# Optimization experiments

Measured on AMD Instinct MI355X. Metric: run time of the kernel, lower is better.

Reference implementation:

```python
import jax, jax.numpy as jnp
import numpy as np
import math

B, T, C, D, E = 4, 2048, 2048, 128, 16

def _xavier(key, shape):
    fan_in, fan_out = shape[-2], shape[-1]
    a = math.sqrt(6.0 / (fan_in + fan_out))
    return jax.random.uniform(key, shape, jnp.float32, -a, a)

def setup_inputs() -> dict:
    key = jax.random.key(0)
    ks = jax.random.split(key, 6)
    return {
        'hidden_states': jax.random.normal(ks[0], (B, T, C), jnp.float32),
        'sim_matrix': jax.random.normal(ks[1], (C, E), jnp.float32),
        'gates': jnp.zeros((E,), jnp.float32),
        'q_proj': _xavier(ks[2], (E, C, D)),
        'k_proj': _xavier(ks[3], (E, C, D)),
        'v_proj': _xavier(ks[4], (E, C, D)),
        'o_proj': _xavier(ks[5], (E, D, C)),
        'min_experts': 2,
    }

def _gating(hidden_states, sim_matrix, gates, min_experts):
    b, t, c = hidden_states.shape
    e = sim_matrix.shape[1]
    x = hidden_states.reshape(b * t, c)
    xn = x / jnp.maximum(jnp.linalg.norm(x, axis=-1, keepdims=True), 1e-12)
    sn = sim_matrix / jnp.maximum(jnp.linalg.norm(sim_matrix, axis=0, keepdims=True), 1e-12)
    logits = xn @ sn - jax.nn.sigmoid(gates)            # [N, E]
    gated = jax.nn.relu(logits)
    # STE: hard threshold forward, identity backward
    hard = (gated > 0).astype(gated.dtype)
    act_mask = gated + jax.lax.stop_gradient(hard - gated)
    inactive = jnp.sum(act_mask, axis=1) == 0           # [N]
    _, fb_idx = jax.lax.top_k(logits, min_experts)      # [N, k]
    fb_mask = jnp.max(jax.nn.one_hot(fb_idx, e, dtype=act_mask.dtype), axis=1)
    act_mask = jnp.where(inactive[:, None], jnp.maximum(act_mask, fb_mask), act_mask)
    masked = jnp.where(act_mask > 0, gated, -jnp.inf)
    routing = jax.nn.softmax(masked, axis=-1)
    return routing.reshape(b, t, e)

def reference(hidden_states, sim_matrix, gates, q_proj, k_proj, v_proj, o_proj, min_experts):
    b, t, c = hidden_states.shape
    rw = _gating(hidden_states, sim_matrix, gates, min_experts)   # [B,T,E]
    # fused: per-expert GEMM then routing-weighted sum (avoids [B,T,D,C] weight tensor)
    q = jnp.einsum('bte,bted->btd', rw, jnp.einsum('btc,ecd->bted', hidden_states, q_proj))
    k = jnp.einsum('bte,bted->btd', rw, jnp.einsum('btc,ecd->bted', hidden_states, k_proj))
    v = jnp.einsum('bte,bted->btd', rw, jnp.einsum('btc,ecd->bted', hidden_states, v_proj))
    scale = 1.0 / math.sqrt(q.shape[-1])
    scores = jnp.einsum('btd,bsd->bts', q, k) * scale
    causal = jnp.tril(jnp.ones((t, t), bool))
    scores = jnp.where(causal[None], scores, -jnp.inf)
    attn = jax.nn.softmax(scores, axis=-1)
    o = jnp.einsum('bts,bsd->btd', attn, v)                       # [B,T,D]
    # output projection: weighted per-expert o_proj applied per token
    out = jnp.einsum('bte,bted->btd'.replace('d','c'), rw, jnp.einsum('btd,edc->btec', o, o_proj))
    return out
```

## Files before the change

### kernel.cpp

```cpp
#include <hip/hip_runtime.h>
#include <hip/hip_bf16.h>

#define DEV __device__ __forceinline__

typedef short bf16x8 __attribute__((ext_vector_type(8)));
typedef float f32x4 __attribute__((ext_vector_type(4)));
typedef unsigned short u16x4 __attribute__((ext_vector_type(4)));

static constexpr int Bsz = 4, Tt = 2048, Cch = 2048, Dd = 128, Ee = 16;
static constexpr int Nn = Bsz * Tt;
static constexpr int CAP = 1280;
static constexpr int MAXTILES = 320;
static constexpr int MT = CAP / 128;
static constexpr int NGRP = MT * Ee;

DEV unsigned short f2bf(float v) {
    __hip_bfloat16 h = __float2bfloat16(v);
    return __builtin_bit_cast(unsigned short, h);
}
DEV float bf2f(unsigned short u) {
    unsigned int x = ((unsigned int)u) << 16;
    return __builtin_bit_cast(float, x);
}

__global__ __launch_bounds__(256) void simt_kernel(const float* __restrict__ sim,
                                                   float* __restrict__ simT) {
    int i = blockIdx.x * 256 + threadIdx.x;
    int e = i >> 11, c = i & 2047;
    simT[i] = sim[c * 16 + e];
}

__global__ __launch_bounds__(1024) void gating6_kernel(
    const float* __restrict__ x, const float* __restrict__ simT,
    const float* __restrict__ gates, const int* __restrict__ minex,
    float* __restrict__ rw, unsigned short* __restrict__ xb,
    int* __restrict__ onmaskv) {
    __shared__ f32x4 ssim[8192];
    __shared__ float snv[16];
    const int tid = threadIdx.x;
    const f32x4* stg = (const f32x4*)simT;
#pragma unroll
    for (int i = 0; i < 8; i++) ssim[i * 1024 + tid] = stg[i * 1024 + tid];
    __syncthreads();
    const int wave = tid >> 6, lane = tid & 63;

    {
        float s = 0.f;
#pragma unroll
        for (int it = 0; it < 8; it++) {
            const f32x4 v = ssim[wave * 512 + it * 64 + lane];
            s += v[0] * v[0] + v[1] * v[1] + v[2] * v[2] + v[3] * v[3];
        }
#pragma unroll
        for (int off = 32; off; off >>= 1) s += __shfl_down(s, off);
        if (lane == 0) snv[wave] = 1.f / fmaxf(sqrtf(s), 1e-12f);
    }
    __syncthreads();

#pragma unroll 1
    for (int g = 0; g < 2; g++) {
        const int n = blockIdx.x * 32 + g * 16 + wave;
        const f32x4* xr = (const f32x4*)(x + (size_t)n * Cch);
        u16x4* xbr = (u16x4*)(xb + (size_t)n * Cch);
        float ss = 0.f;
        float d[16];
#pragma unroll
        for (int e = 0; e < 16; e++) d[e] = 0.f;

#pragma unroll 2
        for (int it = 0; it < 8; it++) {
            const int i = it * 64 + lane;
            const f32x4 xv = xr[i];
            ss += xv[0] * xv[0] + xv[1] * xv[1] + xv[2] * xv[2] + xv[3] * xv[3];
            u16x4 xc = {f2bf(xv[0]), f2bf(xv[1]), f2bf(xv[2]), f2bf(xv[3])};
            xbr[i] = xc;
#pragma unroll
            for (int e = 0; e < 16; e++) {
                const f32x4 sv = ssim[e * 512 + i];
                d[e] += xv[0] * sv[0] + xv[1] * sv[1] + xv[2] * sv[2] + xv[3] * sv[3];
            }
        }
#pragma unroll
        for (int off = 32; off; off >>= 1) {
            ss += __shfl_down(ss, off);
#pragma unroll
            for (int e = 0; e < 16; e++) d[e] += __shfl_down(d[e], off);
        }
        if (lane == 0) {
            float inv = 1.f / fmaxf(sqrtf(ss), 1e-12f);
            float logit[16];
            int onmask = 0;
#pragma unroll
            for (int e = 0; e < 16; e++) {
                float sg = 1.f / (1.f + __expf(-gates[e]));
                float l = d[e] * inv * snv[e] - sg;
                logit[e] = l;
                if (l > 0.f) onmask |= (1 << e);
            }
            if (onmask == 0) {
                int k = *minex;
                int ch = 0;
                for (int kk = 0; kk < k; kk++) {
                    float bv = -1e30f;
                    int be = 0;
#pragma unroll
                    for (int e = 0; e < 16; e++)
                        if (!((ch >> e) & 1) && logit[e] > bv) { bv = logit[e]; be = e; }
                    ch |= (1 << be);
                }
                onmask = ch;
            }
            float mx = -1e30f;
#pragma unroll
            for (int e = 0; e < 16; e++)
                if ((onmask >> e) & 1) mx = fmaxf(mx, fmaxf(logit[e], 0.f));
            float pe[16];
            float sum = 0.f;
#pragma unroll
            for (int e = 0; e < 16; e++) {
                pe[e] = ((onmask >> e) & 1) ? __expf(fmaxf(logit[e], 0.f) - mx) : 0.f;
                sum += pe[e];
            }
            float isum = 1.f / sum;
#pragma unroll
            for (int e = 0; e < 16; e++) rw[(size_t)n * 16 + e] = pe[e] * isum;
            onmaskv[n] = onmask;
        }
    }
}

__global__ __launch_bounds__(256) void scan_fused(
    const int* __restrict__ onmaskv,
    int* __restrict__ idx, int* __restrict__ pos, int* __restrict__ cnt,
    int* __restrict__ ptok, int4* __restrict__ tiledesc, int* __restrict__ ntile_dev,
    int* __restrict__ ocnt, int* __restrict__ olist) {
    const int tid = threadIdx.x;
    const int lane = tid & 63, w = tid >> 6;
    if (blockIdx.x < 16) {
        const int e = blockIdx.x;
        const int base = tid * 32;
        int om[32];
        int c = 0;
#pragma unroll
        for (int i = 0; i < 32; i++) {
            om[i] = (onmaskv[base + i] >> e) & 1;
            c += om[i];
        }
        int sc = c;
#pragma unroll
        for (int off = 1; off < 64; off <<= 1) {
            int t = __shfl_up(sc, off);
            if (lane >= off) sc += t;
        }
        __shared__ int wsum[4];
        if (lane == 63) wsum[w] = sc;
        __syncthreads();
        int wbase = 0;
        for (int i = 0; i < w; i++) wbase += wsum[i];
        int slot = wbase + sc - c;
#pragma unroll
        for (int i = 0; i < 32; i++) {
            int n = base + i;
            int p = -1;
            if (om[i]) {
                if (slot < CAP) {
                    idx[(size_t)e * CAP + slot] = n;
                    p = slot;
                }
                slot++;
            }
            pos[(size_t)n * 16 + e] = p;
        }
        if (tid == 255) cnt[e] = slot;
        return;
    }
    __shared__ int hist[256], cursor[256];
    __shared__ int wsA[4], wsB[4];
    if (tid == 0) *ocnt = 0;
    hist[tid] = 0;
    __syncthreads();
    for (int i = 0; i < 32; i++) {
        int n = tid * 32 + i;
        int m = onmaskv[n];
        if (!m) m = 1;
        int e0 = __ffs(m) - 1;
        int m2 = m & (m - 1);
        int e1 = m2 ? (__ffs(m2) - 1) : e0;
        atomicAdd(&hist[e0 * 16 + e1], 1);
        int mrest = m2 & (m2 - 1);
        while (mrest) {
            int e = __ffs(mrest) - 1;
            int s = atomicAdd(ocnt, 1);
            olist[2 * s] = n;
            olist[2 * s + 1] = e;
            mrest &= (mrest - 1);
        }
    }
    __syncthreads();
    int v = hist[tid];
    int s = v;
#pragma unroll
    for (int off = 1; off < 64; off <<= 1) {
        int t = __shfl_up(s, off);
        if (lane >= off) s += t;
    }
    if (lane == 63) wsA[w] = s;
    __syncthreads();
    int add = 0;
    for (int i = 0; i < w; i++) add += wsA[i];
    int excl = s + add - v;
    cursor[tid] = excl;
    int nt = (v + 127) >> 7;
    int s2 = nt;
#pragma unroll
    for (int off = 1; off < 64; off <<= 1) {
        int t = __shfl_up(s2, off);
        if (lane >= off) s2 += t;
    }
    if (lane == 63) wsB[w] = s2;
    __syncthreads();
    int add2 = 0;
    for (int i = 0; i < w; i++) add2 += wsB[i];
    int texcl = s2 + add2 - nt;
    for (int m = 0; m < nt; m++)
        tiledesc[texcl + m] = make_int4(tid, excl + m * 128, min(128, v - m * 128), 0);
    if (tid == 255) *ntile_dev = texcl + nt;
    __syncthreads();
    for (int i = 0; i < 32; i++) {
        int n = tid * 32 + i;
        int m = onmaskv[n];
        if (!m) m = 1;
        int e0 = __ffs(m) - 1;
        int m2 = m & (m - 1);
        int e1 = m2 ? (__ffs(m2) - 1) : e0;
        int slot = atomicAdd(&cursor[e0 * 16 + e1], 1);
        ptok[slot] = n;
    }
}

__global__ __launch_bounds__(256) void transpose_qkv(
    const float* __restrict__ qp, const float* __restrict__ kp,
    const float* __restrict__ vp, unsigned short* __restrict__ wqkvT) {
    const int z = blockIdx.z;
    const int t3 = z >> 4, e = z & 15;
    const float* src = (t3 == 0 ? qp : (t3 == 1 ? kp : vp)) + (size_t)e * Cch * Dd;
    unsigned short* dst = wqkvT + (size_t)e * 384 * Cch + (size_t)t3 * Dd * Cch;
    __shared__ float tile[32][33];
    int bx = blockIdx.x * 32, by = blockIdx.y * 32;
    int tx = threadIdx.x & 31, ty = threadIdx.x >> 5;
#pragma unroll
    for (int i = 0; i < 4; i++)
        tile[ty + i * 8][tx] = src[(size_t)(by + ty + i * 8) * Dd + bx + tx];
    __syncthreads();
#pragma unroll
    for (int i = 0; i < 4; i++)
        dst[(size_t)(bx + ty + i * 8) * Cch + by + tx] = f2bf(tile[tx][ty + i * 8]);
}

__global__ __launch_bounds__(256) void transpose_f32_bf16(
    const float* __restrict__ src, unsigned short* __restrict__ dst,
    int R, int Ccol, long ss, long ds) {
    __shared__ float tile[32][33];
    src += (size_t)blockIdx.z * ss;
    dst += (size_t)blockIdx.z * ds;
    int bx = blockIdx.x * 32, by = blockIdx.y * 32;
    int tx = threadIdx.x & 31, ty = threadIdx.x >> 5;
#pragma unroll
    for (int i = 0; i < 4; i++)
        tile[ty + i * 8][tx] = src[(size_t)(by + ty + i * 8) * Ccol + bx + tx];
    __syncthreads();
#pragma unroll
    for (int i = 0; i < 4; i++)
        dst[(size_t)(bx + ty + i * 8) * R + by + tx] = f2bf(tile[tx][ty + i * 8]);
}

__global__ __launch_bounds__(256) void transpose_u16(
    const unsigned short* __restrict__ src, unsigned short* __restrict__ dst,
    int R, int Ccol, long ss, long ds) {
    __shared__ unsigned short tile[32][33];
    src += (size_t)blockIdx.z * ss;
    dst += (size_t)blockIdx.z * ds;
    int bx = blockIdx.x * 32, by = blockIdx.y * 32;
    int tx = threadIdx.x & 31, ty = threadIdx.x >> 5;
#pragma unroll
    for (int i = 0; i < 4; i++)
        tile[ty + i * 8][tx] = src[(size_t)(by + ty + i * 8) * Ccol + bx + tx];
    __syncthreads();
#pragma unroll
    for (int i = 0; i < 4; i++)
        dst[(size_t)(bx + ty + i * 8) * R + by + tx] = tile[tx][ty + i * 8];
}

__global__ __launch_bounds__(256) void gemm_qkv_gather(
    const unsigned short* __restrict__ X, const unsigned short* __restrict__ W,
    const int* __restrict__ idx, const int* __restrict__ cnt,
    unsigned short* __restrict__ P) {
    const int L = blockIdx.x;
    const int r = L & 7, s = L >> 3;
    const int gq = s / 3, j = s - gq * 3;
    const int g = gq * 8 + r;
    const int m = g % MT;
    const int e = g / MT;
    const int cn = min(cnt[e], CAP);
    const int bm = m * 128;
    if (bm >= cn) return;
    const int bn = j * 128;
    __shared__ alignas(16) unsigned short As[2 * 128 * 64];
    __shared__ alignas(16) unsigned short Bs[2 * 128 * 64];
    __shared__ int toks[128];
    const int tid = threadIdx.x;
    if (tid < 128) toks[tid] = idx[(size_t)e * CAP + min(bm + tid, cn - 1)];
    const unsigned short* Wb = W + ((size_t)e * 384 + bn) * Cch;
    const int wave = tid >> 6, lane = tid & 63;
    const int lr = lane & 15, lg = lane >> 4;
    const int wr = (wave >> 1) * 64, wc = (wave & 1) * 64;
    f32x4 acc[4][4] = {};

    auto stage = [&](int buf, int k0) {
#pragma unroll
        for (int i = 0; i < 4; i++) {
            int t = i * 256 + tid;
            int row = t >> 3;
            int kc = (t & 7) << 3;
            __builtin_amdgcn_global_load_lds(
                (const __attribute__((address_space(1))) void*)(X + (size_t)toks[row] * Cch + k0 + kc),
                (__attribute__((address_space(3))) void*)(As + buf * 8192 + (i * 4 + wave) * 512),
                16, 0, 0);
        }
#pragma unroll
        for (int i = 0; i < 4; i++) {
            int t = i * 256 + tid;
            int row = t >> 3;
            int kc = (t & 7) << 3;
            __builtin_amdgcn_global_load_lds(
                (const __attribute__((address_space(1))) void*)(Wb + (size_t)row * Cch + k0 + kc),
                (__attribute__((address_space(3))) void*)(Bs + buf * 8192 + (i * 4 + wave) * 512),
                16, 0, 0);
        }
    };

    __syncthreads();
    stage(0, 0);
    __syncthreads();
    int cur = 0;
#pragma unroll 1
    for (int t = 0; t < 32; t++) {
        if (t + 1 < 32) stage(cur ^ 1, (t + 1) * 64);
        const unsigned short* Ab = As + cur * 8192;
        const unsigned short* Bb = Bs + cur * 8192;
#pragma unroll
        for (int kk = 0; kk < 2; kk++) {
            bf16x8 a[4], b[4];
#pragma unroll
            for (int m2 = 0; m2 < 4; m2++)
                a[m2] = *(const bf16x8*)(Ab + (wr + m2 * 16 + lr) * 64 + kk * 32 + lg * 8);
#pragma unroll
            for (int n = 0; n < 4; n++)
                b[n] = *(const bf16x8*)(Bb + (wc + n * 16 + lr) * 64 + kk * 32 + lg * 8);
#pragma unroll
            for (int m2 = 0; m2 < 4; m2++)
#pragma unroll
                for (int n = 0; n < 4; n++)
                    acc[m2][n] = __builtin_amdgcn_mfma_f32_16x16x32_bf16(a[m2], b[n], acc[m2][n], 0, 0, 0);
        }
        __syncthreads();
        cur ^= 1;
    }
#pragma unroll
    for (int m2 = 0; m2 < 4; m2++)
#pragma unroll
        for (int n = 0; n < 4; n++)
#pragma unroll
            for (int rr = 0; rr < 4; rr++) {
                int slot = bm + wr + m2 * 16 + lg * 4 + rr;
                int col = bn + wc + n * 16 + lr;
                if (slot < cn)
                    P[((size_t)e * CAP + slot) * 384 + col] = f2bf(acc[m2][n][rr]);
            }
}

__global__ __launch_bounds__(256) void combine_qkv(
    const unsigned short* __restrict__ P, const float* __restrict__ rw,
    const int* __restrict__ pos,
    unsigned short* __restrict__ qb, unsigned short* __restrict__ kb,
    unsigned short* __restrict__ vb) {
    int i = blockIdx.x * 256 + threadIdx.x;
    int n = i >> 5;
    int d4 = (i & 31) << 2;
    float aq[4] = {}, ak[4] = {}, av[4] = {};
#pragma unroll
    for (int e = 0; e < 16; e++) {
        int p = pos[(size_t)n * 16 + e];
        if (p >= 0) {
            float w = rw[(size_t)n * 16 + e];
            const unsigned short* rh = P + ((size_t)e * CAP + p) * 384 + d4;
            const u16x4 q4 = *(const u16x4*)(rh);
            const u16x4 k4 = *(const u16x4*)(rh + 128);
            const u16x4 v4 = *(const u16x4*)(rh + 256);
#pragma unroll
            for (int jj = 0; jj < 4; jj++) {
                aq[jj] += w * bf2f(q4[jj]);
                ak[jj] += w * bf2f(k4[jj]);
                av[jj] += w * bf2f(v4[jj]);
            }
        }
    }
    u16x4 sq = {f2bf(aq[0]), f2bf(aq[1]), f2bf(aq[2]), f2bf(aq[3])};
    u16x4 sk = {f2bf(ak[0]), f2bf(ak[1]), f2bf(ak[2]), f2bf(ak[3])};
    u16x4 sv = {f2bf(av[0]), f2bf(av[1]), f2bf(av[2]), f2bf(av[3])};
    *(u16x4*)(qb + (size_t)n * Dd + d4) = sq;
    *(u16x4*)(kb + (size_t)n * Dd + d4) = sk;
    *(u16x4*)(vb + (size_t)n * Dd + d4) = sv;
}

__global__ __launch_bounds__(256) void flash_kernel(
    const unsigned short* __restrict__ qb, const unsigned short* __restrict__ kb,
    const unsigned short* __restrict__ vT,
    float* __restrict__ Op, float* __restrict__ ml) {
    const int qt = blockIdx.x, ch = blockIdx.y, b = blockIdx.z;
    const int q0 = qt * 128, kv0 = ch * 512;
    if (kv0 > q0 + 127) return;
    __shared__ alignas(16) unsigned short Qs[128 * 128];
    __shared__ alignas(16) unsigned short Ks[64 * 128];
    __shared__ alignas(16) unsigned short Vs[128 * 64];
    __shared__ alignas(16) unsigned short Ps[4][32 * 64];
    const int tid = threadIdx.x;
    const int wave = tid >> 6, lane = tid & 63;
    const int lr = lane & 15, lg = lane >> 4;
    const float scale = 0.08838834764831845f;
    const unsigned short* Qg = qb + ((size_t)b * Tt + q0) * 128;
    const unsigned short* Kg = kb + (size_t)b * Tt * 128;
    const unsigned short* Vg = vT + (size_t)b * 128 * Tt;

#pragma unroll
    for (int i = 0; i < 8; i++) {
        int dof = (i * 256 + tid) << 4;
        int row = dof >> 8;
        int c16 = (dof >> 4) & 15;
        int s16 = c16 ^ (row & 7);
        __builtin_amdgcn_global_load_lds(
            (const __attribute__((address_space(1))) void*)(Qg + (size_t)row * 128 + s16 * 8),
            (__attribute__((address_space(3))) void*)(Qs + (size_t)(i * 4 + wave) * 512),
            16, 0, 0);
    }

    f32x4 acc_o[2][8] = {};
    float rm[2][4], rl[2][4];
#pragma unroll
    for (int mf = 0; mf < 2; mf++)
#pragma unroll
        for (int rg = 0; rg < 4; rg++) { rm[mf][rg] = -1e30f; rl[mf][rg] = 0.f; }

    const int ktend = min(kv0 + 512, q0 + 128);
    for (int kt = kv0; kt < ktend; kt += 64) {
        if (kt > kv0) __syncthreads();
#pragma unroll
        for (int i = 0; i < 4; i++) {
            int dof = (i * 256 + tid) << 4;
            int row = dof >> 8;
            int c16 = (dof >> 4) & 15;
            int s16 = c16 ^ (row & 7);
            __builtin_amdgcn_global_load_lds(
                (const __attribute__((address_space(1))) void*)(Kg + (size_t)(kt + row) * 128 + s16 * 8),
                (__attribute__((address_space(3))) void*)(Ks + (size_t)(i * 4 + wave) * 512),
                16, 0, 0);
        }
#pragma unroll
        for (int i = 0; i < 4; i++) {
            int dof = (i * 256 + tid) << 4;
            int row = dof >> 7;
            int c16 = (dof >> 4) & 7;
            int s16 = c16 ^ (row & 7);
            __builtin_amdgcn_global_load_lds(
                (const __attribute__((address_space(1))) void*)(Vg + (size_t)row * Tt + kt + s16 * 8),
                (__attribute__((address_space(3))) void*)(Vs + (size_t)(i * 4 + wave) * 512),
                16, 0, 0);
        }
        __syncthreads();

        f32x4 acc_s[2][4] = {};
#pragma unroll
        for (int kk = 0; kk < 4; kk++) {
            bf16x8 a[2], bfr[4];
#pragma unroll
            for (int mf = 0; mf < 2; mf++) {
                int row = wave * 32 + mf * 16 + lr;
                int c16 = (kk * 4 + lg) ^ (row & 7);
                a[mf] = *(const bf16x8*)(Qs + row * 128 + c16 * 8);
            }
#pragma unroll
            for (int nf = 0; nf < 4; nf++) {
                int row = nf * 16 + lr;
                int c16 = (kk * 4 + lg) ^ (row & 7);
                bfr[nf] = *(const bf16x8*)(Ks + row * 128 + c16 * 8);
            }
#pragma unroll
            for (int mf = 0; mf < 2; mf++)
#pragma unroll
                for (int nf = 0; nf < 4; nf++)
                    acc_s[mf][nf] = __builtin_amdgcn_mfma_f32_16x16x32_bf16(a[mf], bfr[nf], acc_s[mf][nf], 0, 0, 0);
        }

#pragma unroll
        for (int mf = 0; mf < 2; mf++) {
            float sv[4][4], pmax[4];
#pragma unroll
            for (int rg = 0; rg < 4; rg++) pmax[rg] = -1e30f;
#pragma unroll
            for (int nf = 0; nf < 4; nf++) {
                int colg = kt + nf * 16 + lr;
#pragma unroll
                for (int rg = 0; rg < 4; rg++) {
                    int rowg = q0 + wave * 32 + mf * 16 + lg * 4 + rg;
                    float s = acc_s[mf][nf][rg] * scale;
                    if (colg > rowg) s = -1e30f;
                    sv[nf][rg] = s;
                    pmax[rg] = fmaxf(pmax[rg], s);
                }
            }
#pragma unroll
            for (int rg = 0; rg < 4; rg++) {
#pragma unroll
                for (int off = 1; off < 16; off <<= 1)
                    pmax[rg] = fmaxf(pmax[rg], __shfl_xor(pmax[rg], off));
                float mnew = fmaxf(rm[mf][rg], pmax[rg]);
                float f = __expf(rm[mf][rg] - mnew);
                rm[mf][rg] = mnew;
#pragma unroll
                for (int nd = 0; nd < 8; nd++) acc_o[mf][nd][rg] *= f;
                float rsum = 0.f;
#pragma unroll
                for (int nf = 0; nf < 4; nf++) {
                    float p = __expf(sv[nf][rg] - mnew);
                    sv[nf][rg] = p;
                    rsum += p;
                }
#pragma unroll
                for (int off = 1; off < 16; off <<= 1) rsum += __shfl_xor(rsum, off);
                rl[mf][rg] = rl[mf][rg] * f + rsum;
                int rloc = mf * 16 + lg * 4 + rg;
#pragma unroll
                for (int nf = 0; nf < 4; nf++) {
                    int col = nf * 16 + lr;
                    int unit = (col >> 3) ^ (rloc & 7);
                    Ps[wave][rloc * 64 + unit * 8 + (col & 7)] = f2bf(sv[nf][rg]);
                }
            }
        }

#pragma unroll
        for (int kk2 = 0; kk2 < 2; kk2++) {
            bf16x8 a[2], bfr[8];
#pragma unroll
            for (int mf = 0; mf < 2; mf++) {
                int row = mf * 16 + lr;
                int c16 = (kk2 * 4 + lg) ^ (row & 7);
                a[mf] = *(const bf16x8*)(&Ps[wave][row * 64 + c16 * 8]);
            }
#pragma unroll
            for (int nd = 0; nd < 8; nd++) {
                int row = nd * 16 + lr;
                int c16 = ((kk2 * 4 + lg) ^ (row & 7)) & 7;
                bfr[nd] = *(const bf16x8*)(Vs + row * 64 + c16 * 8);
            }
#pragma unroll
            for (int mf = 0; mf < 2; mf++)
#pragma unroll
                for (int nd = 0; nd < 8; nd++)
                    acc_o[mf][nd] = __builtin_amdgcn_mfma_f32_16x16x32_bf16(a[mf], bfr[nd], acc_o[mf][nd], 0, 0, 0);
        }
    }

    float* Opb = Op + (((size_t)b * 4 + ch) * Tt) * 128;
    float* mlb = ml + (((size_t)b * 4 + ch) * Tt) * 2;
#pragma unroll
    for (int mf = 0; mf < 2; mf++)
#pragma unroll
        for (int rg = 0; rg < 4; rg++) {
            int rowl = q0 + wave * 32 + mf * 16 + lg * 4 + rg;
#pragma unroll
            for (int nd = 0; nd < 8; nd++)
                Opb[(size_t)rowl * 128 + nd * 16 + lr] = acc_o[mf][nd][rg];
            if (lr == 0) {
                mlb[rowl * 2] = rm[mf][rg];
                mlb[rowl * 2 + 1] = rl[mf][rg];
            }
        }
}

__global__ __launch_bounds__(256) void flash_combine(
    const float* __restrict__ Op, const float* __restrict__ ml,
    const float* __restrict__ rw, const int* __restrict__ onmaskv,
    float* __restrict__ ob, unsigned short* __restrict__ og2) {
    int i = blockIdx.x * 256 + threadIdx.x;
    int n = i >> 7, d = i & 127;
    int rs = n & 2047, b = n >> 11;
    int nch = rs / 512 + 1;
    float ms = -1e30f;
    for (int c = 0; c < nch; c++)
        ms = fmaxf(ms, ml[(((size_t)b * 4 + c) * Tt + rs) * 2]);
    float num = 0.f, den = 0.f;
    for (int c = 0; c < nch; c++) {
        size_t rbase = ((size_t)b * 4 + c) * Tt + rs;
        float mi = ml[rbase * 2], li = ml[rbase * 2 + 1];
        float w = __expf(mi - ms);
        num += w * Op[rbase * 128 + d];
        den += w * li;
    }
    float o = num / den;
    ob[(size_t)n * 128 + d] = o;
    int m = onmaskv[n];
    if (!m) m = 1;
    int e0 = __ffs(m) - 1;
    int m2 = m & (m - 1);
    float w0 = rw[(size_t)n * 16 + e0];
    float w1 = m2 ? rw[(size_t)n * 16 + (__ffs(m2) - 1)] : 0.f;
    og2[(size_t)n * 256 + d] = f2bf(w0 * o);
    og2[(size_t)n * 256 + 128 + d] = f2bf(w1 * o);
}

__global__ __launch_bounds__(256) void gemm_pair(
    const unsigned short* __restrict__ og2,
    const unsigned short* __restrict__ woT,
    const int* __restrict__ ptok, const int4* __restrict__ tiledesc,
    const int* __restrict__ ntile_dev,
    float* __restrict__ out) {
    const int L = blockIdx.x;
    const int r = L & 7, s = L >> 3;
    const int bnidx = s & 15, tq = s >> 4;
    const int tile = tq * 8 + r;
    if (tile >= *ntile_dev) return;
    const int4 td = tiledesc[tile];
    const int ei = td.x >> 4, ej = td.x & 15;
    const int mstart = td.y, mcnt = td.z;
    const int bn = bnidx * 128;
    __shared__ alignas(16) unsigned short As[128 * 64];
    __shared__ alignas(16) unsigned short Bs[128 * 64];
    __shared__ int toks[128];
    const int tid = threadIdx.x;
    if (tid < 128) toks[tid] = ptok[mstart + min(tid, mcnt - 1)];
    const int wave = tid >> 6, lane = tid & 63;
    const int lr = lane & 15, lg = lane >> 4;
    const int wr = (wave >> 1) * 64, wc = (wave & 1) * 64;
    f32x4 acc[4][4] = {};

#pragma unroll
    for (int ck = 0; ck < 4; ck++) {
        const int ebase = (ck < 2 ? ei : ej) * 128 + (ck & 1) * 64;
        const int abase = ck * 64;
        __syncthreads();
#pragma unroll
        for (int q = 0; q < 4; q++) {
            int t = q * 256 + tid;
            int row = t >> 3;
            int kc = (t & 7) << 3;
            __builtin_amdgcn_global_load_lds(
                (const __attribute__((address_space(1))) void*)(og2 + (size_t)toks[row] * 256 + abase + kc),
                (__attribute__((address_space(3))) void*)(As + (q * 4 + wave) * 512),
                16, 0, 0);
        }
#pragma unroll
        for (int q = 0; q < 4; q++) {
            int t = q * 256 + tid;
            int row = t >> 3;
            int kc = (t & 7) << 3;
            __builtin_amdgcn_global_load_lds(
                (const __attribute__((address_space(1))) void*)(woT + (size_t)(bn + row) * 2048 + ebase + kc),
                (__attribute__((address_space(3))) void*)(Bs + (q * 4 + wave) * 512),
                16, 0, 0);
        }
        __syncthreads();
#pragma unroll
        for (int kk = 0; kk < 2; kk++) {
            bf16x8 a[4], b[4];
#pragma unroll
            for (int m = 0; m < 4; m++)
                a[m] = *(const bf16x8*)(As + (wr + m * 16 + lr) * 64 + kk * 32 + lg * 8);
#pragma unroll
            for (int n = 0; n < 4; n++)
                b[n] = *(const bf16x8*)(Bs + (wc + n * 16 + lr) * 64 + kk * 32 + lg * 8);
#pragma unroll
            for (int m = 0; m < 4; m++)
#pragma unroll
                for (int n = 0; n < 4; n++)
                    acc[m][n] = __builtin_amdgcn_mfma_f32_16x16x32_bf16(a[m], b[n], acc[m][n], 0, 0, 0);
        }
    }
#pragma unroll
    for (int m = 0; m < 4; m++)
#pragma unroll
        for (int n = 0; n < 4; n++)
#pragma unroll
            for (int rr2 = 0; rr2 < 4; rr2++) {
                int rowt = wr + m * 16 + lg * 4 + rr2;
                if (rowt < mcnt) {
                    int tok = toks[rowt];
                    out[(size_t)tok * 2048 + bn + wc + n * 16 + lr] = acc[m][n][rr2];
                }
            }
}

__global__ __launch_bounds__(256) void overflow_kernel(
    const int* __restrict__ ocnt, const int* __restrict__ olist,
    const float* __restrict__ ob, const unsigned short* __restrict__ woT,
    const float* __restrict__ rw, float* __restrict__ out) {
    const int ne = *ocnt;
    __shared__ float osh[128];
    for (int it = blockIdx.x; it < ne; it += gridDim.x) {
        int n = olist[2 * it], e = olist[2 * it + 1];
        float wgt = rw[(size_t)n * 16 + e];
        if (threadIdx.x < 128) osh[threadIdx.x] = ob[(size_t)n * Dd + threadIdx.x];
        __syncthreads();
#pragma unroll 1
        for (int cc = 0; cc < 8; cc++) {
            int c = threadIdx.x * 8 + cc;
            float a = 0.f;
            for (int k = 0; k < 128; k++)
                a += osh[k] * bf2f(woT[(size_t)c * 2048 + e * 128 + k]);
            atomicAdd(&out[(size_t)n * 2048 + c], wgt * a);
        }
        __syncthreads();
    }
}

extern "C" void kernel_launch(void* const* d_in, const int* in_sizes, int n_in,
                              void* d_out, int out_size, void* d_ws, size_t ws_size,
                              hipStream_t stream) {
    (void)in_sizes; (void)n_in; (void)out_size; (void)ws_size;
    const float* hidden = (const float*)d_in[0];
    const float* sim = (const float*)d_in[1];
    const float* gates = (const float*)d_in[2];
    const float* qp = (const float*)d_in[3];
    const float* kp = (const float*)d_in[4];
    const float* vp = (const float*)d_in[5];
    const float* op = (const float*)d_in[6];
    const int* minex = (const int*)d_in[7];
    float* out = (float*)d_out;

    char* w = (char*)d_ws;
    size_t off = 0;
    auto alloc = [&](size_t bytes) -> char* {
        char* p = w + off;
        off = (off + bytes + 255) & ~(size_t)255;
        return p;
    };
    unsigned short* xb = (unsigned short*)alloc((size_t)Nn * Cch * 2);
    unsigned short* wqkvT = (unsigned short*)alloc((size_t)Ee * 384 * Cch * 2);
    unsigned short* woT = (unsigned short*)alloc((size_t)Cch * Ee * Dd * 2);
    float* rw = (float*)alloc((size_t)Nn * Ee * 4);
    float* simT = (float*)alloc((size_t)Ee * Cch * 4);
    int* cnt = (int*)alloc(256);
    int* onmaskv = (int*)alloc((size_t)Nn * 4);
    int* idx = (int*)alloc((size_t)Ee * CAP * 4);
    int* pos = (int*)alloc((size_t)Nn * 16 * 4);
    int* ptok = (int*)alloc((size_t)Nn * 4);
    int4* tiledesc = (int4*)alloc((size_t)MAXTILES * 16);
    int* ntile_dev = (int*)alloc(256);
    int* ocnt = (int*)alloc(256);
    int* olist = (int*)alloc((size_t)Nn * 14 * 2 * 4);
    char* big = alloc((size_t)Bsz * Tt * Tt * 4);
    unsigned short* qb = (unsigned short*)alloc((size_t)Nn * Dd * 2);
    unsigned short* kb = (unsigned short*)alloc((size_t)Nn * Dd * 2);
    unsigned short* vb = (unsigned short*)alloc((size_t)Nn * Dd * 2);
    unsigned short* vT = (unsigned short*)alloc((size_t)Bsz * Dd * Tt * 2);
    float* ob = (float*)alloc((size_t)Nn * Dd * 4);
    unsigned short* og2 = (unsigned short*)alloc((size_t)Nn * 256 * 2);
    float* ml = (float*)alloc((size_t)Bsz * 4 * Tt * 2 * 4);
    unsigned short* Pc = (unsigned short*)big;
    float* Op = (float*)big;

    simt_kernel<<<(Ee * Cch) / 256, 256, 0, stream>>>(sim, simT);
    gating6_kernel<<<Nn / 32, 1024, 0, stream>>>(hidden, simT, gates, minex, rw, xb, onmaskv);
    scan_fused<<<17, 256, 0, stream>>>(onmaskv, idx, pos, cnt, ptok, tiledesc, ntile_dev, ocnt, olist);

    transpose_qkv<<<dim3(Dd / 32, Cch / 32, 48), 256, 0, stream>>>(qp, kp, vp, wqkvT);
    transpose_f32_bf16<<<dim3((Ee * Dd) / 32, Cch / 32, 1), 256, 0, stream>>>(
        op, woT, Ee * Dd, Cch, 0L, 0L);

    gemm_qkv_gather<<<NGRP * 3, 256, 0, stream>>>(xb, wqkvT, idx, cnt, Pc);
    combine_qkv<<<(Nn * 32) / 256, 256, 0, stream>>>(Pc, rw, pos, qb, kb, vb);

    transpose_u16<<<dim3(Dd / 32, Tt / 32, Bsz), 256, 0, stream>>>(
        vb, vT, Tt, Dd, (long)Tt * Dd, (long)Dd * Tt);

    flash_kernel<<<dim3(Tt / 128, 4, Bsz), 256, 0, stream>>>(qb, kb, vT, Op, ml);
    flash_combine<<<(Nn * 128) / 256, 256, 0, stream>>>(Op, ml, rw, onmaskv, ob, og2);

    gemm_pair<<<MAXTILES * 16, 256, 0, stream>>>(
        og2, woT, ptok, tiledesc, ntile_dev, out);
    overflow_kernel<<<256, 256, 0, stream>>>(ocnt, olist, ob, woT, rw, out);
}
```

Measured before the change: 238.8 us.

## Swizzle LDS tiles in gather GEMMs, remap QKV blocks, process two tokens per wave

The gating kernel now has each wave handle two consecutive tokens at once, so every shared-memory sim load feeds two dot products. The gather QKV GEMM and the pair GEMM XOR-swizzle the 16-byte column chunks, both on the global-to-LDS load and on the MFMA fragment reads. This is meant to avoid LDS bank conflicts. The QKV block index mapping is also reorganised so that blocks sharing an expert and a row tile run close together, which should improve reuse of X and W in cache. The costs are more live registers in gating and some extra index arithmetic.

Result: faster. 222.2 us (-7.0%).

```diff
diff --git a/kernel.cpp b/kernel.cpp
--- a/kernel.cpp
+++ b/kernel.cpp
@@ -30,7 +30,7 @@
     simT[i] = sim[c * 16 + e];
 }
 
-__global__ __launch_bounds__(1024) void gating6_kernel(
+__global__ __launch_bounds__(1024) void gating7_kernel(
     const float* __restrict__ x, const float* __restrict__ simT,
     const float* __restrict__ gates, const int* __restrict__ minex,
     float* __restrict__ rw, unsigned short* __restrict__ xb,
@@ -57,43 +57,56 @@
     }
     __syncthreads();
 
+    const int n0 = blockIdx.x * 32 + wave * 2;
+    const f32x4* xr0 = (const f32x4*)(x + (size_t)n0 * Cch);
+    const f32x4* xr1 = (const f32x4*)(x + (size_t)(n0 + 1) * Cch);
+    u16x4* xb0 = (u16x4*)(xb + (size_t)n0 * Cch);
+    u16x4* xb1 = (u16x4*)(xb + (size_t)(n0 + 1) * Cch);
+    float ss[2] = {0.f, 0.f};
+    float d[2][16];
+#pragma unroll
+    for (int t = 0; t < 2; t++)
+#pragma unroll
+        for (int e = 0; e < 16; e++) d[t][e] = 0.f;
+
+#pragma unroll 2
+    for (int it = 0; it < 8; it++) {
+        const int i = it * 64 + lane;
+        const f32x4 xv0 = xr0[i];
+        const f32x4 xv1 = xr1[i];
+        ss[0] += xv0[0] * xv0[0] + xv0[1] * xv0[1] + xv0[2] * xv0[2] + xv0[3] * xv0[3];
+        ss[1] += xv1[0] * xv1[0] + xv1[1] * xv1[1] + xv1[2] * xv1[2] + xv1[3] * xv1[3];
+        u16x4 c0 = {f2bf(xv0[0]), f2bf(xv0[1]), f2bf(xv0[2]), f2bf(xv0[3])};
+        u16x4 c1 = {f2bf(xv1[0]), f2bf(xv1[1]), f2bf(xv1[2]), f2bf(xv1[3])};
+        xb0[i] = c0;
+        xb1[i] = c1;
+#pragma unroll
+        for (int e = 0; e < 16; e++) {
+            const f32x4 sv = ssim[e * 512 + i];
+            d[0][e] += xv0[0] * sv[0] + xv0[1] * sv[1] + xv0[2] * sv[2] + xv0[3] * sv[3];
+            d[1][e] += xv1[0] * sv[0] + xv1[1] * sv[1] + xv1[2] * sv[2] + xv1[3] * sv[3];
+        }
+    }
+#pragma unroll
+    for (int off = 32; off; off >>= 1) {
+#pragma unroll
+        for (int t = 0; t < 2; t++) {
+            ss[t] += __shfl_down(ss[t], off);
+#pragma unroll
+            for (int e = 0; e < 16; e++) d[t][e] += __shfl_down(d[t][e], off);
+        }
+    }
+    if (lane == 0) {
 #pragma unroll 1
-    for (int g = 0; g < 2; g++) {
-        const int n = blockIdx.x * 32 + g * 16 + wave;
-        const f32x4* xr = (const f32x4*)(x + (size_t)n * Cch);
-        u16x4* xbr = (u16x4*)(xb + (size_t)n * Cch);
-        float ss = 0.f;
-        float d[16];
-#pragma unroll
-        for (int e = 0; e < 16; e++) d[e] = 0.f;
-
-#pragma unroll 2
-        for (int it = 0; it < 8; it++) {
-            const int i = it * 64 + lane;
-            const f32x4 xv = xr[i];
-            ss += xv[0] * xv[0] + xv[1] * xv[1] + xv[2] * xv[2] + xv[3] * xv[3];
-            u16x4 xc = {f2bf(xv[0]), f2bf(xv[1]), f2bf(xv[2]), f2bf(xv[3])};
-            xbr[i] = xc;
-#pragma unroll
-            for (int e = 0; e < 16; e++) {
-                const f32x4 sv = ssim[e * 512 + i];
-                d[e] += xv[0] * sv[0] + xv[1] * sv[1] + xv[2] * sv[2] + xv[3] * sv[3];
-            }
-        }
-#pragma unroll
-        for (int off = 32; off; off >>= 1) {
-            ss += __shfl_down(ss, off);
-#pragma unroll
-            for (int e = 0; e < 16; e++) d[e] += __shfl_down(d[e], off);
-        }
-        if (lane == 0) {
-            float inv = 1.f / fmaxf(sqrtf(ss), 1e-12f);
+        for (int t = 0; t < 2; t++) {
+            const int n = n0 + t;
+            float inv = 1.f / fmaxf(sqrtf(ss[t]), 1e-12f);
             float logit[16];
             int onmask = 0;
 #pragma unroll
             for (int e = 0; e < 16; e++) {
                 float sg = 1.f / (1.f + __expf(-gates[e]));
-                float l = d[e] * inv * snv[e] - sg;
+                float l = d[t][e] * inv * snv[e] - sg;
                 logit[e] = l;
                 if (l > 0.f) onmask |= (1 << e);
             }
@@ -296,11 +309,11 @@
     const int* __restrict__ idx, const int* __restrict__ cnt,
     unsigned short* __restrict__ P) {
     const int L = blockIdx.x;
-    const int r = L & 7, s = L >> 3;
-    const int gq = s / 3, j = s - gq * 3;
-    const int g = gq * 8 + r;
-    const int m = g % MT;
-    const int e = g / MT;
+    const int r = L & 7, i5 = L >> 3;
+    const int e = r * 2 + (i5 / 30);
+    const int rem = i5 % 30;
+    const int m = rem % MT;
+    const int j = rem / MT;
     const int cn = min(cnt[e], CAP);
     const int bm = m * 128;
     if (bm >= cn) return;
@@ -321,9 +334,9 @@
         for (int i = 0; i < 4; i++) {
             int t = i * 256 + tid;
             int row = t >> 3;
-            int kc = (t & 7) << 3;
+            int sc = (t & 7) ^ (row & 7);
             __builtin_amdgcn_global_load_lds(
-                (const __attribute__((address_space(1))) void*)(X + (size_t)toks[row] * Cch + k0 + kc),
+                (const __attribute__((address_space(1))) void*)(X + (size_t)toks[row] * Cch + k0 + sc * 8),
                 (__attribute__((address_space(3))) void*)(As + buf * 8192 + (i * 4 + wave) * 512),
                 16, 0, 0);
         }
@@ -331,9 +344,9 @@
         for (int i = 0; i < 4; i++) {
             int t = i * 256 + tid;
             int row = t >> 3;
-            int kc = (t & 7) << 3;
+            int sc = (t & 7) ^ (row & 7);
             __builtin_amdgcn_global_load_lds(
-                (const __attribute__((address_space(1))) void*)(Wb + (size_t)row * Cch + k0 + kc),
+                (const __attribute__((address_space(1))) void*)(Wb + (size_t)row * Cch + k0 + sc * 8),
                 (__attribute__((address_space(3))) void*)(Bs + buf * 8192 + (i * 4 + wave) * 512),
                 16, 0, 0);
         }
@@ -352,11 +365,17 @@
         for (int kk = 0; kk < 2; kk++) {
             bf16x8 a[4], b[4];
 #pragma unroll
-            for (int m2 = 0; m2 < 4; m2++)
-                a[m2] = *(const bf16x8*)(Ab + (wr + m2 * 16 + lr) * 64 + kk * 32 + lg * 8);
-#pragma unroll
-            for (int n = 0; n < 4; n++)
-                b[n] = *(const bf16x8*)(Bb + (wc + n * 16 + lr) * 64 + kk * 32 + lg * 8);
+            for (int m2 = 0; m2 < 4; m2++) {
+                int row = wr + m2 * 16 + lr;
+                int u = (kk * 4 + lg) ^ (row & 7);
+                a[m2] = *(const bf16x8*)(Ab + row * 64 + u * 8);
+            }
+#pragma unroll
+            for (int n = 0; n < 4; n++) {
+                int row = wc + n * 16 + lr;
+                int u = (kk * 4 + lg) ^ (row & 7);
+                b[n] = *(const bf16x8*)(Bb + row * 64 + u * 8);
+            }
 #pragma unroll
             for (int m2 = 0; m2 < 4; m2++)
 #pragma unroll
@@ -653,9 +672,9 @@
         for (int q = 0; q < 4; q++) {
             int t = q * 256 + tid;
             int row = t >> 3;
-            int kc = (t & 7) << 3;
+            int sc = (t & 7) ^ (row & 7);
             __builtin_amdgcn_global_load_lds(
-                (const __attribute__((address_space(1))) void*)(og2 + (size_t)toks[row] * 256 + abase + kc),
+                (const __attribute__((address_space(1))) void*)(og2 + (size_t)toks[row] * 256 + abase + sc * 8),
                 (__attribute__((address_space(3))) void*)(As + (q * 4 + wave) * 512),
                 16, 0, 0);
         }
@@ -663,9 +682,9 @@
         for (int q = 0; q < 4; q++) {
             int t = q * 256 + tid;
             int row = t >> 3;
-            int kc = (t & 7) << 3;
+            int sc = (t & 7) ^ (row & 7);
             __builtin_amdgcn_global_load_lds(
-                (const __attribute__((address_space(1))) void*)(woT + (size_t)(bn + row) * 2048 + ebase + kc),
+                (const __attribute__((address_space(1))) void*)(woT + (size_t)(bn + row) * 2048 + ebase + sc * 8),
                 (__attribute__((address_space(3))) void*)(Bs + (q * 4 + wave) * 512),
                 16, 0, 0);
         }
@@ -674,11 +693,17 @@
         for (int kk = 0; kk < 2; kk++) {
             bf16x8 a[4], b[4];
 #pragma unroll
-            for (int m = 0; m < 4; m++)
-                a[m] = *(const bf16x8*)(As + (wr + m * 16 + lr) * 64 + kk * 32 + lg * 8);
-#pragma unroll
-            for (int n = 0; n < 4; n++)
-                b[n] = *(const bf16x8*)(Bs + (wc + n * 16 + lr) * 64 + kk * 32 + lg * 8);
+            for (int m = 0; m < 4; m++) {
+                int row = wr + m * 16 + lr;
+                int u = (kk * 4 + lg) ^ (row & 7);
+                a[m] = *(const bf16x8*)(As + row * 64 + u * 8);
+            }
+#pragma unroll
+            for (int n = 0; n < 4; n++) {
+                int row = wc + n * 16 + lr;
+                int u = (kk * 4 + lg) ^ (row & 7);
+                b[n] = *(const bf16x8*)(Bs + row * 64 + u * 8);
+            }
 #pragma unroll
             for (int m = 0; m < 4; m++)
 #pragma unroll
@@ -770,7 +795,7 @@
     float* Op = (float*)big;
 
     simt_kernel<<<(Ee * Cch) / 256, 256, 0, stream>>>(sim, simT);
-    gating6_kernel<<<Nn / 32, 1024, 0, stream>>>(hidden, simT, gates, minex, rw, xb, onmaskv);
+    gating7_kernel<<<Nn / 32, 1024, 0, stream>>>(hidden, simT, gates, minex, rw, xb, onmaskv);
     scan_fused<<<17, 256, 0, stream>>>(onmaskv, idx, pos, cnt, ptok, tiledesc, ntile_dev, ocnt, olist);
 
     transpose_qkv<<<dim3(Dd / 32, Cch / 32, 48), 256, 0, stream>>>(qp, kp, vp, wqkvT);
```
